# Kernel tuning notes

Hardware: AMD Instinct MI355X
Metric: run time of the kernel (lower is better)

Reference implementation:

```python
import jax, jax.numpy as jnp
import numpy as np

B, S, T = 16, 1024, 512
D, H, L, FF = 256, 8, 4, 1024
DH = D // H  # 32, even (RoPE requirement)


def setup_inputs() -> dict:
    key = jax.random.key(0)
    ks = jax.random.split(key, 8)
    n = lambda k, shape: jax.random.normal(k, shape, dtype=jnp.float32) * 0.02
    return {
        "x": jax.random.normal(ks[0], (B, S, T), dtype=jnp.float32),
        "tok_w": n(ks[1], (D, T)), "tok_b": jnp.zeros((D,), jnp.float32),
        "tnorm_g": jnp.ones((D,), jnp.float32), "tnorm_b": jnp.zeros((D,), jnp.float32),
        "in_proj_w": n(ks[2], (L, 3 * D, D)), "in_proj_b": jnp.zeros((L, 3 * D), jnp.float32),
        "out_w": n(ks[3], (L, D, D)), "out_b": jnp.zeros((L, D), jnp.float32),
        "ln1_g": jnp.ones((L, D), jnp.float32), "ln1_b": jnp.zeros((L, D), jnp.float32),
        "ln2_g": jnp.ones((L, D), jnp.float32), "ln2_b": jnp.zeros((L, D), jnp.float32),
        "lin1_w": n(ks[4], (L, FF, D)), "lin1_b": jnp.zeros((L, FF), jnp.float32),
        "lin2_w": n(ks[5], (L, D, FF)), "lin2_b": jnp.zeros((L, D), jnp.float32),
        "fnorm_g": jnp.ones((D,), jnp.float32), "fnorm_b": jnp.zeros((D,), jnp.float32),
    }


def _ln(x, g, b, eps=1e-5):
    m = x.mean(-1, keepdims=True)
    v = ((x - m) ** 2).mean(-1, keepdims=True)
    return (x - m) * jax.lax.rsqrt(v + eps) * g + b


def _rope_cache():
    half = DH // 2
    inv_freq = 1.0 / (10000.0 ** (jnp.arange(half, dtype=jnp.float32) / half))
    freqs = jnp.arange(S, dtype=jnp.float32)[:, None] * inv_freq[None, :]  # (S, half)
    cos = jnp.concatenate([jnp.cos(freqs), jnp.cos(freqs)], axis=-1)  # (S, DH)
    sin = jnp.concatenate([jnp.sin(freqs), jnp.sin(freqs)], axis=-1)
    return cos[None, None], sin[None, None]  # (1,1,S,DH)


def _rotate_half(x):
    x1, x2 = jnp.split(x, 2, axis=-1)
    return jnp.concatenate([-x2, x1], axis=-1)


def _rope(x, cos, sin):
    return x * cos + _rotate_half(x) * sin


def _encoder(x, tok_w, tok_b, tnorm_g, tnorm_b, in_proj_w, in_proj_b,
             out_w, out_b, ln1_g, ln1_b, ln2_g, ln2_b,
             lin1_w, lin1_b, lin2_w, lin2_b, fnorm_g, fnorm_b):
    # tokenize: Linear(T -> D) per sensor, then LayerNorm
    h = _ln(x @ tok_w.T + tok_b, tnorm_g, tnorm_b)  # (B,S,D)
    cos, sin = _rope_cache()
    scale = 1.0 / np.sqrt(DH).astype(np.float32)
    for i in range(L):
        # --- pre-norm RoPE self-attention ---
        y = _ln(h, ln1_g[i], ln1_b[i])
        qkv = y @ in_proj_w[i].T + in_proj_b[i]  # (B,S,3D)
        q, k, v = jnp.split(qkv, 3, axis=-1)
        q = q.reshape(B, S, H, DH).transpose(0, 2, 1, 3)  # (B,H,S,DH)
        k = k.reshape(B, S, H, DH).transpose(0, 2, 1, 3)
        v = v.reshape(B, S, H, DH).transpose(0, 2, 1, 3)
        q = _rope(q, cos, sin)
        k = _rope(k, cos, sin)
        attn = jax.nn.softmax(jnp.einsum('bhqd,bhkd->bhqk', q, k) * scale, axis=-1)
        o = jnp.einsum('bhqk,bhkd->bhqd', attn, v)
        o = o.transpose(0, 2, 1, 3).reshape(B, S, D)
        h = h + o @ out_w[i].T + out_b[i]
        # --- pre-norm FFN ---
        y2 = _ln(h, ln2_g[i], ln2_b[i])
        h = h + jax.nn.relu(y2 @ lin1_w[i].T + lin1_b[i]) @ lin2_w[i].T + lin2_b[i]
    return _ln(h, fnorm_g, fnorm_b)


def reference(x, tok_w, tok_b, tnorm_g, tnorm_b, in_proj_w, in_proj_b,
              out_w, out_b, ln1_g, ln1_b, ln2_g, ln2_b,
              lin1_w, lin1_b, lin2_w, lin2_b, fnorm_g, fnorm_b):
    return _encoder(x, tok_w, tok_b, tnorm_g, tnorm_b, in_proj_w, in_proj_b,
                    out_w, out_b, ln1_g, ln1_b, ln2_g, ln2_b,
                    lin1_w, lin1_b, lin2_w, lin2_b, fnorm_g, fnorm_b)
```

## Files before the change

kernel.cpp:

```cpp
#include <hip/hip_runtime.h>

#define BB 16
#define SS 1024
#define TT 512
#define DD 256
#define HH 8
#define LL 4
#define FFN 1024
#define DHH 32
#define MROWS (BB*SS)

typedef short bf16x8 __attribute__((ext_vector_type(8)));
typedef float f32x4 __attribute__((ext_vector_type(4)));
typedef float f32x2 __attribute__((ext_vector_type(2)));
typedef unsigned int u32x4 __attribute__((ext_vector_type(4)));

__device__ __forceinline__ unsigned short f2bf(float f) {
    unsigned int u = __float_as_uint(f);
    unsigned int r = (u + 0x7fffu + ((u >> 16) & 1u)) >> 16;
    return (unsigned short)r;
}
__device__ __forceinline__ float bf2f(unsigned short h) {
    return __uint_as_float(((unsigned int)h) << 16);
}
__device__ __forceinline__ unsigned int packbf(float a, float b) {
    return (__float_as_uint(a) >> 16) | (__float_as_uint(b) & 0xffff0000u);
}
__device__ __forceinline__ unsigned int packbf_perm(float p0, float p1) {
    return __builtin_amdgcn_perm(__float_as_uint(p1), __float_as_uint(p0), 0x07060302u);
}

__device__ __forceinline__ void g2l16(const unsigned short* g, unsigned short* l) {
    __builtin_amdgcn_global_load_lds(
        (const __attribute__((address_space(1))) unsigned int*)g,
        (__attribute__((address_space(3))) unsigned int*)l, 16, 0, 0);
}

__global__ __launch_bounds__(256) void convert_weights(
    const float* __restrict__ w0, const float* __restrict__ w1, const float* __restrict__ w2,
    const float* __restrict__ w3, const float* __restrict__ w4, unsigned short* __restrict__ dst)
{
    int i = blockIdx.x * 256 + threadIdx.x;
    if (i >= 3276800) return;
    float v;
    if (i < 131072)        v = w0[i];
    else if (i < 917504)   v = w1[i - 131072];
    else if (i < 1179648)  v = w2[i - 917504];
    else if (i < 2228224)  v = w3[i - 1179648];
    else                   v = w4[i - 2228224];
    dst[i] = f2bf(v);
}

__global__ __launch_bounds__(256) void convert_x(const float4* __restrict__ x, ushort4* __restrict__ xb, int n4)
{
    int i = blockIdx.x * 256 + threadIdx.x;
    if (i >= n4) return;
    float4 v = x[i];
    ushort4 o;
    o.x = f2bf(v.x); o.y = f2bf(v.y); o.z = f2bf(v.z); o.w = f2bf(v.w);
    xb[i] = o;
}

template<int BN, int RELU>
__global__ __launch_bounds__(256, 2) void gemm_lds(
    const unsigned short* __restrict__ A, const unsigned short* __restrict__ Bw,
    const float* __restrict__ bias, void* out, int M, int N, int K)
{
    constexpr int NJ = BN / 32;
    __shared__ __align__(16) unsigned short sA[2][128 * 32];
    __shared__ __align__(16) unsigned short sB[2][BN * 32];
    const int t = threadIdx.x;
    const int lane = t & 63, quad = lane >> 4, l16 = lane & 15;
    const int wave = t >> 6, wm = wave >> 1, wn = wave & 1;
    const int row0 = blockIdx.y * 128, col0 = blockIdx.x * BN;

    const unsigned short* gA = A + (size_t)(row0 + (t >> 2)) * K + (t & 3) * 8;
    const size_t rstep = (size_t)64 * K;
    const unsigned short* gBp[BN / 64];
    #pragma unroll
    for (int p = 0; p < BN / 64; ++p) {
        int l = p * 64 + (t >> 2);
        int wrow = (l & (16 * NJ)) + (l & 15) * NJ + ((l >> 4) & (NJ - 1));
        gBp[p] = Bw + (size_t)(col0 + wrow) * K + (t & 3) * 8;
    }

    f32x4 acc[4][NJ];
    #pragma unroll
    for (int i = 0; i < 4; ++i)
        #pragma unroll
        for (int j = 0; j < NJ; ++j)
            acc[i][j] = (f32x4){0.f, 0.f, 0.f, 0.f};

    g2l16(gA, &sA[0][t * 8]);
    g2l16(gA + rstep, &sA[0][(t + 256) * 8]);
    #pragma unroll
    for (int p = 0; p < BN / 64; ++p)
        g2l16(gBp[p], &sB[0][p * 2048 + t * 8]);

    for (int k0 = 0; k0 < K; k0 += 32) {
        const int cur = (k0 >> 5) & 1;
        __syncthreads();
        if (k0 + 32 < K) {
            const int nxt = cur ^ 1;
            g2l16(gA + k0 + 32, &sA[nxt][t * 8]);
            g2l16(gA + rstep + k0 + 32, &sA[nxt][(t + 256) * 8]);
            #pragma unroll
            for (int p = 0; p < BN / 64; ++p)
                g2l16(gBp[p] + k0 + 32, &sB[nxt][p * 2048 + t * 8]);
        }
        bf16x8 a[4], b[NJ];
        #pragma unroll
        for (int i = 0; i < 4; ++i)
            a[i] = *(const bf16x8*)(&sA[cur][(wm * 64 + i * 16 + l16) * 32 + quad * 8]);
        #pragma unroll
        for (int j = 0; j < NJ; ++j)
            b[j] = *(const bf16x8*)(&sB[cur][(wn * (BN / 2) + j * 16 + l16) * 32 + quad * 8]);
        #pragma unroll
        for (int i = 0; i < 4; ++i)
            #pragma unroll
            for (int j = 0; j < NJ; ++j)
                acc[i][j] = __builtin_amdgcn_mfma_f32_16x16x32_bf16(a[i], b[j], acc[i][j], 0, 0, 0);
    }

    const int colbase = col0 + wn * (BN / 2) + l16 * NJ;
    float bb[NJ];
    #pragma unroll
    for (int j = 0; j < NJ; ++j) bb[j] = bias[colbase + j];
    #pragma unroll
    for (int i = 0; i < 4; ++i) {
        #pragma unroll
        for (int r = 0; r < 4; ++r) {
            int row = row0 + wm * 64 + i * 16 + quad * 4 + r;
            float v[NJ];
            #pragma unroll
            for (int j = 0; j < NJ; ++j) {
                v[j] = acc[i][j][r] + bb[j];
                if (RELU) v[j] = fmaxf(v[j], 0.f);
            }
            unsigned short* dst = (unsigned short*)out + (size_t)row * N + colbase;
            if constexpr (NJ == 4) {
                uint2 w; w.x = packbf(v[0], v[1]); w.y = packbf(v[2], v[3]);
                *(uint2*)dst = w;
            } else {
                uint4 w; w.x = packbf(v[0], v[1]); w.y = packbf(v[2], v[3]);
                w.z = packbf(v[4], v[5]); w.w = packbf(v[6], v[7]);
                *(uint4*)dst = w;
            }
        }
    }
}

template<int RESID, int LNH, int YF32>
__global__ __launch_bounds__(512, 2) void gemm_row(
    const unsigned short* __restrict__ A, const unsigned short* __restrict__ Bw,
    const float* __restrict__ bias, const float* __restrict__ resid,
    float* __restrict__ hout, void* __restrict__ yout,
    const float* __restrict__ gh, const float* __restrict__ bh,
    const float* __restrict__ gy, const float* __restrict__ by, int K)
{
    __shared__ __align__(16) unsigned short sA[2][64 * 32];
    __shared__ __align__(16) unsigned short sB[2][256 * 32];
    __shared__ float2 part[2][64][4];
    const int t = threadIdx.x;
    const int quad = (t >> 4) & 3, l16 = t & 15;
    const int wave = t >> 6, wm = wave >> 2, wn = wave & 3;
    const int row0 = blockIdx.x * 64;

    const unsigned short* gA = A + (size_t)(row0 + ((t >> 2) & 63)) * K + (t & 3) * 8;
    const int l0 = t >> 2, l1 = 128 + l0;
    const unsigned short* gB0 = Bw + (size_t)((l0 & 192) + (l0 & 15) * 4 + ((l0 >> 4) & 3)) * K + (t & 3) * 8;
    const unsigned short* gB1 = Bw + (size_t)((l1 & 192) + (l1 & 15) * 4 + ((l1 >> 4) & 3)) * K + (t & 3) * 8;

    f32x4 acc[2][4];
    #pragma unroll
    for (int i = 0; i < 2; ++i)
        #pragma unroll
        for (int j = 0; j < 4; ++j)
            acc[i][j] = (f32x4){0.f, 0.f, 0.f, 0.f};

    auto stage = [&](int k0, int buf) {
        if (t < 256) g2l16(gA + k0, &sA[buf][t * 8]);
        g2l16(gB0 + k0, &sB[buf][t * 8]);
        g2l16(gB1 + k0, &sB[buf][(t + 512) * 8]);
    };

    stage(0, 0);
    for (int k0 = 0; k0 < K; k0 += 32) {
        const int cur = (k0 >> 5) & 1;
        __syncthreads();
        if (k0 + 32 < K) stage(k0 + 32, cur ^ 1);
        bf16x8 a[2], b[4];
        #pragma unroll
        for (int i = 0; i < 2; ++i)
            a[i] = *(const bf16x8*)(&sA[cur][(wm * 32 + i * 16 + l16) * 32 + quad * 8]);
        #pragma unroll
        for (int j = 0; j < 4; ++j)
            b[j] = *(const bf16x8*)(&sB[cur][(wn * 64 + j * 16 + l16) * 32 + quad * 8]);
        #pragma unroll
        for (int i = 0; i < 2; ++i)
            #pragma unroll
            for (int j = 0; j < 4; ++j)
                acc[i][j] = __builtin_amdgcn_mfma_f32_16x16x32_bf16(a[i], b[j], acc[i][j], 0, 0, 0);
    }

    const int colbase = wn * 64 + l16 * 4;
    const float4 bb = *(const float4*)(bias + colbase);
    #pragma unroll
    for (int i = 0; i < 2; ++i) {
        #pragma unroll
        for (int r = 0; r < 4; ++r) {
            const int rl = wm * 32 + i * 16 + quad * 4 + r;
            float v0 = acc[i][0][r] + bb.x;
            float v1 = acc[i][1][r] + bb.y;
            float v2 = acc[i][2][r] + bb.z;
            float v3 = acc[i][3][r] + bb.w;
            if (RESID) {
                float4 rv = *(const float4*)(resid + (size_t)(row0 + rl) * DD + colbase);
                v0 += rv.x; v1 += rv.y; v2 += rv.z; v3 += rv.w;
            }
            acc[i][0][r] = v0; acc[i][1][r] = v1; acc[i][2][r] = v2; acc[i][3][r] = v3;
            float s = v0 + v1 + v2 + v3;
            float ss = v0 * v0 + v1 * v1 + v2 * v2 + v3 * v3;
            #pragma unroll
            for (int m = 1; m <= 8; m <<= 1) { s += __shfl_xor(s, m); ss += __shfl_xor(ss, m); }
            if (l16 == 0) part[0][rl][wn] = (float2){s, ss};
        }
    }
    __syncthreads();

    float4 gyv = *(const float4*)(gy + colbase);
    float4 byv = *(const float4*)(by + colbase);
    float4 ghv = {0.f, 0.f, 0.f, 0.f}, bhv = {0.f, 0.f, 0.f, 0.f};
    if (LNH) { ghv = *(const float4*)(gh + colbase); bhv = *(const float4*)(bh + colbase); }

    #pragma unroll
    for (int i = 0; i < 2; ++i) {
        #pragma unroll
        for (int r = 0; r < 4; ++r) {
            const int rl = wm * 32 + i * 16 + quad * 4 + r;
            float2 p0 = part[0][rl][0], p1 = part[0][rl][1], p2 = part[0][rl][2], p3 = part[0][rl][3];
            float mean = (p0.x + p1.x + p2.x + p3.x) * (1.f / 256.f);
            float var  = (p0.y + p1.y + p2.y + p3.y) * (1.f / 256.f) - mean * mean;
            float inv  = rsqrtf(var + 1e-5f);
            float h0, h1, h2, h3;
            if (LNH) {
                h0 = (acc[i][0][r] - mean) * inv * ghv.x + bhv.x;
                h1 = (acc[i][1][r] - mean) * inv * ghv.y + bhv.y;
                h2 = (acc[i][2][r] - mean) * inv * ghv.z + bhv.z;
                h3 = (acc[i][3][r] - mean) * inv * ghv.w + bhv.w;
            } else {
                h0 = acc[i][0][r]; h1 = acc[i][1][r]; h2 = acc[i][2][r]; h3 = acc[i][3][r];
            }
            if (!YF32)
                *(float4*)(hout + (size_t)(row0 + rl) * DD + colbase) = (float4){h0, h1, h2, h3};
            if (LNH) {
                acc[i][0][r] = h0; acc[i][1][r] = h1; acc[i][2][r] = h2; acc[i][3][r] = h3;
                float s = h0 + h1 + h2 + h3;
                float ss = h0 * h0 + h1 * h1 + h2 * h2 + h3 * h3;
                #pragma unroll
                for (int m = 1; m <= 8; m <<= 1) { s += __shfl_xor(s, m); ss += __shfl_xor(ss, m); }
                if (l16 == 0) part[1][rl][wn] = (float2){s, ss};
            } else {
                float y0 = (h0 - mean) * inv * gyv.x + byv.x;
                float y1 = (h1 - mean) * inv * gyv.y + byv.y;
                float y2 = (h2 - mean) * inv * gyv.z + byv.z;
                float y3 = (h3 - mean) * inv * gyv.w + byv.w;
                if (YF32) {
                    *(float4*)((float*)yout + (size_t)(row0 + rl) * DD + colbase) = (float4){y0, y1, y2, y3};
                } else {
                    uint2 w; w.x = packbf(y0, y1); w.y = packbf(y2, y3);
                    *(uint2*)((unsigned short*)yout + (size_t)(row0 + rl) * DD + colbase) = w;
                }
            }
        }
    }

    if (LNH) {
        __syncthreads();
        #pragma unroll
        for (int i = 0; i < 2; ++i) {
            #pragma unroll
            for (int r = 0; r < 4; ++r) {
                const int rl = wm * 32 + i * 16 + quad * 4 + r;
                float2 p0 = part[1][rl][0], p1 = part[1][rl][1], p2 = part[1][rl][2], p3 = part[1][rl][3];
                float mean = (p0.x + p1.x + p2.x + p3.x) * (1.f / 256.f);
                float var  = (p0.y + p1.y + p2.y + p3.y) * (1.f / 256.f) - mean * mean;
                float inv  = rsqrtf(var + 1e-5f);
                float y0 = (acc[i][0][r] - mean) * inv * gyv.x + byv.x;
                float y1 = (acc[i][1][r] - mean) * inv * gyv.y + byv.y;
                float y2 = (acc[i][2][r] - mean) * inv * gyv.z + byv.z;
                float y3 = (acc[i][3][r] - mean) * inv * gyv.w + byv.w;
                uint2 w; w.x = packbf(y0, y1); w.y = packbf(y2, y3);
                *(uint2*)((unsigned short*)yout + (size_t)(row0 + rl) * DD + colbase) = w;
            }
        }
    }
}

__global__ __launch_bounds__(512) void rope_kernel(const unsigned short* __restrict__ qkv,
    unsigned short* __restrict__ qr, unsigned short* __restrict__ kr, unsigned short* __restrict__ vt)
{
    __shared__ float scc[64 * 16], scs[64 * 16];
    __shared__ unsigned short vlds[256 * 68];
    const int t = threadIdx.x;
    const int r0 = blockIdx.x * 64;
    const int b = r0 >> 10, s0 = r0 & 1023;

    #pragma unroll
    for (int e2 = 0; e2 < 2; ++e2) {
        int e = t * 2 + e2;
        int rl = e >> 4, jj = e & 15;
        float ivf = __expf(-(float)jj * 0.575646273248511f);
        float c, sn;
        __sincosf((float)(s0 + rl) * ivf, &sn, &c);
        scc[rl * 16 + jj] = c;
        scs[rl * 16 + jj] = sn;
    }
    __syncthreads();

    const int sub = t >> 8, i = t & 255;
    const int h = i >> 5, d = i & 31, j = d & 15;
    const int bh = (b << 3) | h;
    const float qscale = 1.4426950408889634f / 5.656854249492381f;
    for (int it = 0; it < 32; ++it) {
        int rl = it * 2 + sub;
        int s = s0 + rl;
        const unsigned short* rp = qkv + (size_t)(r0 + rl) * 768;
        float qv = bf2f(rp[i]);
        float kv = bf2f(rp[256 + i]);
        float vv = bf2f(rp[512 + i]);
        float c = scc[rl * 16 + j], sn = scs[rl * 16 + j];
        float qp = __shfl_xor(qv, 16);
        float kp = __shfl_xor(kv, 16);
        float rq = (qv * c + ((d < 16) ? -qp : qp) * sn) * qscale;
        float rk = kv * c + ((d < 16) ? -kp : kp) * sn;
        qr[((size_t)bh * SS + s) * DHH + d] = f2bf(rq);
        int jj2 = s & 31;
        int sp = (s & ~31) | (((jj2 & 1) << 4) | (jj2 >> 1));
        kr[((size_t)bh * SS + sp) * DHH + d] = f2bf(rk);
        vlds[i * 68 + rl] = f2bf(vv);
    }
    __syncthreads();

    const int wave = t >> 6, lane = t & 63;
    for (int p = 0; p < 32; ++p) {
        int row = p * 8 + wave;
        int hh = row >> 5, dd = row & 31;
        unsigned short v = vlds[row * 68 + lane];
        vt[((size_t)((b << 3) | hh) * DHH + dd) * SS + s0 + lane] = v;
    }
}

__global__ __launch_bounds__(128, 2) void attn_kernel(
    const unsigned short* __restrict__ qr, const unsigned short* __restrict__ kr,
    const unsigned short* __restrict__ vt, unsigned short* __restrict__ ob)
{
    int t = threadIdx.x;
    int lane = t & 63, wave = t >> 6;
    int quad = (lane >> 4), l16 = lane & 15;
    int bid = blockIdx.x;
    int xcd = bid & 7, jb = bid >> 3;
    int gid = jb * 2 + wave;
    int bh = xcd * 16 + (gid >> 4);
    int q0 = (gid & 15) * 64;
    int b = bh >> 3, h = bh & 7;
    const unsigned short* qbase = qr + ((size_t)bh * SS + q0) * DHH;
    const unsigned short* kbase = kr + (size_t)bh * SS * DHH;
    const unsigned short* vbase = vt + (size_t)bh * DHH * SS;
    bf16x8 qa[4];
    #pragma unroll
    for (int qt = 0; qt < 4; ++qt)
        qa[qt] = *(const bf16x8*)(qbase + (size_t)(qt * 16 + l16) * DHH + quad * 8);
    f32x4 o[4][2] = {};
    f32x2 lsum[4] = {};

    bf16x8 kbA[2][2], vbA[2][2], kbB[2][2], vbB[2][2];

    auto loadKV = [&](int k0, bf16x8 (&kb)[2][2], bf16x8 (&vb)[2][2]) {
        #pragma unroll
        for (int kc = 0; kc < 2; ++kc) {
            const unsigned short* kp = kbase + (size_t)(k0 + kc * 32) * DHH;
            kb[kc][0] = *(const bf16x8*)(kp + (size_t)l16 * DHH + quad * 8);
            kb[kc][1] = *(const bf16x8*)(kp + (size_t)(16 + l16) * DHH + quad * 8);
            vb[kc][0] = *(const bf16x8*)(vbase + (size_t)l16 * SS + k0 + kc * 32 + quad * 8);
            vb[kc][1] = *(const bf16x8*)(vbase + (size_t)(l16 + 16) * SS + k0 + kc * 32 + quad * 8);
        }
    };

    auto tile = [&](bf16x8 (&kb)[2][2], bf16x8 (&vb)[2][2]) {
        __builtin_amdgcn_s_setprio(1);
        #pragma unroll
        for (int qt = 0; qt < 4; ++qt)
            #pragma unroll
            for (int kc = 0; kc < 2; ++kc) {
                f32x4 z = {0.f, 0.f, 0.f, 0.f};
                f32x4 s0 = __builtin_amdgcn_mfma_f32_16x16x32_bf16(kb[kc][0], qa[qt], z, 0, 0, 0);
                f32x4 s1 = __builtin_amdgcn_mfma_f32_16x16x32_bf16(kb[kc][1], qa[qt], z, 0, 0, 0);
                u32x4 pw;
                #pragma unroll
                for (int r = 0; r < 4; ++r) {
                    float p0 = __builtin_amdgcn_exp2f(s0[r]);
                    float p1 = __builtin_amdgcn_exp2f(s1[r]);
                    lsum[qt] += (f32x2){p0, p1};
                    pw[r] = packbf_perm(p0, p1);
                }
                bf16x8 pa = __builtin_bit_cast(bf16x8, pw);
                o[qt][0] = __builtin_amdgcn_mfma_f32_16x16x32_bf16(pa, vb[kc][0], o[qt][0], 0, 0, 0);
                o[qt][1] = __builtin_amdgcn_mfma_f32_16x16x32_bf16(pa, vb[kc][1], o[qt][1], 0, 0, 0);
            }
        __builtin_amdgcn_s_setprio(0);
    };

    loadKV(0, kbA, vbA);
    for (int k0 = 0; k0 < SS; k0 += 128) {
        loadKV(k0 + 64, kbB, vbB);
        tile(kbA, vbA);
        if (k0 + 128 < SS) loadKV(k0 + 128, kbA, vbA);
        tile(kbB, vbB);
    }

    #pragma unroll
    for (int qt = 0; qt < 4; ++qt) {
        float s = lsum[qt][0] + lsum[qt][1];
        s += __shfl_xor(s, 16);
        s += __shfl_xor(s, 32);
        float inv = 1.f / s;
        #pragma unroll
        for (int r = 0; r < 4; ++r) {
            float invr = __shfl(inv, quad * 4 + r);
            int qrow = q0 + qt * 16 + quad * 4 + r;
            size_t base = ((size_t)b * SS + qrow) * DD + h * DHH;
            ob[base + l16]      = f2bf(o[qt][0][r] * invr);
            ob[base + 16 + l16] = f2bf(o[qt][1][r] * invr);
        }
    }
}

extern "C" void kernel_launch(void* const* d_in, const int* in_sizes, int n_in,
                              void* d_out, int out_size, void* d_ws, size_t ws_size,
                              hipStream_t stream)
{
    const float* x        = (const float*)d_in[0];
    const float* tok_w    = (const float*)d_in[1];
    const float* tok_b    = (const float*)d_in[2];
    const float* tnorm_g  = (const float*)d_in[3];
    const float* tnorm_b  = (const float*)d_in[4];
    const float* in_proj_w= (const float*)d_in[5];
    const float* in_proj_b= (const float*)d_in[6];
    const float* out_w    = (const float*)d_in[7];
    const float* out_b    = (const float*)d_in[8];
    const float* ln1_g    = (const float*)d_in[9];
    const float* ln1_b    = (const float*)d_in[10];
    const float* ln2_g    = (const float*)d_in[11];
    const float* ln2_b    = (const float*)d_in[12];
    const float* lin1_w   = (const float*)d_in[13];
    const float* lin1_b   = (const float*)d_in[14];
    const float* lin2_w   = (const float*)d_in[15];
    const float* lin2_b   = (const float*)d_in[16];
    const float* fnorm_g  = (const float*)d_in[17];
    const float* fnorm_b  = (const float*)d_in[18];

    char* ws = (char*)d_ws;
    unsigned short* wb        = (unsigned short*)ws;
    unsigned short* wb_tok    = wb;
    unsigned short* wb_inproj = wb + 131072;
    unsigned short* wb_out    = wb + 917504;
    unsigned short* wb_lin1   = wb + 1179648;
    unsigned short* wb_lin2   = wb + 2228224;
    unsigned short* qkvb = (unsigned short*)(ws + 6553600);
    unsigned short* xb   = qkvb;
    float*          h    = (float*)(ws + 31719424);
    unsigned short* y    = (unsigned short*)(ws + 48496640);
    unsigned short* qr   = (unsigned short*)(ws + 56885248);
    unsigned short* kr   = (unsigned short*)(ws + 65273856);
    unsigned short* vt   = (unsigned short*)(ws + 73662464);
    unsigned short* ob   = (unsigned short*)(ws + 82051072);
    unsigned short* a1   = (unsigned short*)(ws + 90439680);

    convert_weights<<<dim3(12800), dim3(256), 0, stream>>>(tok_w, in_proj_w, out_w, lin1_w, lin2_w, wb);
    convert_x<<<dim3(8192), dim3(256), 0, stream>>>((const float4*)x, (ushort4*)xb, MROWS * TT / 4);

    gemm_row<0, 1, 0><<<dim3(MROWS / 64), dim3(512), 0, stream>>>(
        xb, wb_tok, tok_b, nullptr, h, y, tnorm_g, tnorm_b, ln1_g, ln1_b, TT);

    for (int i = 0; i < LL; ++i) {
        gemm_lds<128, 0><<<dim3((3 * DD) / 128, MROWS / 128), dim3(256), 0, stream>>>(
            y, wb_inproj + (size_t)i * 3 * DD * DD, in_proj_b + i * 3 * DD, qkvb, MROWS, 3 * DD, DD);
        rope_kernel<<<dim3(MROWS / 64), dim3(512), 0, stream>>>(qkvb, qr, kr, vt);
        attn_kernel<<<dim3(1024), dim3(128), 0, stream>>>(qr, kr, vt, ob);
        gemm_row<1, 0, 0><<<dim3(MROWS / 64), dim3(512), 0, stream>>>(
            ob, wb_out + (size_t)i * DD * DD, out_b + i * DD, h, h, y,
            nullptr, nullptr, ln2_g + i * DD, ln2_b + i * DD, DD);
        gemm_lds<256, 1><<<dim3(FFN / 256, MROWS / 128), dim3(256), 0, stream>>>(
            y, wb_lin1 + (size_t)i * FFN * DD, lin1_b + i * FFN, a1, MROWS, FFN, DD);
        if (i < LL - 1) {
            gemm_row<1, 0, 0><<<dim3(MROWS / 64), dim3(512), 0, stream>>>(
                a1, wb_lin2 + (size_t)i * DD * FFN, lin2_b + i * DD, h, h, y,
                nullptr, nullptr, ln1_g + (i + 1) * DD, ln1_b + (i + 1) * DD, FFN);
        } else {
            gemm_row<1, 0, 1><<<dim3(MROWS / 64), dim3(512), 0, stream>>>(
                a1, wb_lin2 + (size_t)i * DD * FFN, lin2_b + i * DD, h, h, d_out,
                nullptr, nullptr, fnorm_g, fnorm_b, FFN);
        }
    }
}
```

Baseline: 608.2 us.

## Fuse RoPE and head-layout scatter into the QKV projection GEMM epilogue

Replaces the separate QKV GEMM plus rope_kernel with a single gemm_qkv kernel. Its B-row permutation lets each lane hold a RoPE pair partner reachable by a shuffle, and the epilogue writes rotated, scaled Q, permuted K and transposed V directly. This removes the write and re-read of the 16k x 768 bf16 qkv buffer and one launch per layer. In exchange the V transpose is now written with strided global stores instead of through LDS, and the GEMM carries extra shared memory for sin/cos tables.

```diff
diff --git a/kernel.cpp b/kernel.cpp
--- a/kernel.cpp
+++ b/kernel.cpp
@@ -145,6 +145,144 @@
                 uint4 w; w.x = packbf(v[0], v[1]); w.y = packbf(v[2], v[3]);
                 w.z = packbf(v[4], v[5]); w.w = packbf(v[6], v[7]);
                 *(uint4*)dst = w;
+            }
+        }
+    }
+}
+
+__global__ __launch_bounds__(256, 2) void gemm_qkv(
+    const unsigned short* __restrict__ A, const unsigned short* __restrict__ Bw,
+    const float* __restrict__ bias,
+    unsigned short* __restrict__ qr, unsigned short* __restrict__ kr,
+    unsigned short* __restrict__ vt)
+{
+    constexpr int K = 256;
+    __shared__ __align__(16) unsigned short sA[2][128 * 32];
+    __shared__ __align__(16) unsigned short sB[2][128 * 32];
+    __shared__ float scc[128 * 20], scs[128 * 20];
+    const int t = threadIdx.x;
+    const int lane = t & 63, quad = lane >> 4, l16 = lane & 15;
+    const int wave = t >> 6, wm = wave >> 1, wn = wave & 1;
+    const int row0 = blockIdx.y * 128, col0 = blockIdx.x * 128;
+    const int sec = blockIdx.x >> 1;
+    const int b = row0 >> 10, s0 = row0 & 1023;
+
+    if (sec < 2) {
+        #pragma unroll
+        for (int k = 0; k < 8; ++k) {
+            int e = t * 8 + k;
+            int rl = e >> 4, jj = e & 15;
+            float ivf = __expf(-(float)jj * 0.575646273248511f);
+            float c, sn;
+            __sincosf((float)(s0 + rl) * ivf, &sn, &c);
+            scc[rl * 20 + jj] = c;
+            scs[rl * 20 + jj] = sn;
+        }
+    }
+
+    const unsigned short* gA = A + (size_t)(row0 + (t >> 2)) * K + (t & 3) * 8;
+    const size_t rstep = (size_t)64 * K;
+    const unsigned short* gBp[2];
+    #pragma unroll
+    for (int p = 0; p < 2; ++p) {
+        int l = p * 64 + (t >> 2);
+        int wrow = (l & 64) + (l & 15) * 4 + ((l >> 4) & 3);
+        gBp[p] = Bw + (size_t)(col0 + wrow) * K + (t & 3) * 8;
+    }
+
+    f32x4 acc[4][4];
+    #pragma unroll
+    for (int i = 0; i < 4; ++i)
+        #pragma unroll
+        for (int j = 0; j < 4; ++j)
+            acc[i][j] = (f32x4){0.f, 0.f, 0.f, 0.f};
+
+    g2l16(gA, &sA[0][t * 8]);
+    g2l16(gA + rstep, &sA[0][(t + 256) * 8]);
+    #pragma unroll
+    for (int p = 0; p < 2; ++p)
+        g2l16(gBp[p], &sB[0][p * 2048 + t * 8]);
+
+    for (int k0 = 0; k0 < K; k0 += 32) {
+        const int cur = (k0 >> 5) & 1;
+        __syncthreads();
+        if (k0 + 32 < K) {
+            const int nxt = cur ^ 1;
+            g2l16(gA + k0 + 32, &sA[nxt][t * 8]);
+            g2l16(gA + rstep + k0 + 32, &sA[nxt][(t + 256) * 8]);
+            #pragma unroll
+            for (int p = 0; p < 2; ++p)
+                g2l16(gBp[p] + k0 + 32, &sB[nxt][p * 2048 + t * 8]);
+        }
+        bf16x8 a[4], bfr[4];
+        #pragma unroll
+        for (int i = 0; i < 4; ++i)
+            a[i] = *(const bf16x8*)(&sA[cur][(wm * 64 + i * 16 + l16) * 32 + quad * 8]);
+        #pragma unroll
+        for (int j = 0; j < 4; ++j)
+            bfr[j] = *(const bf16x8*)(&sB[cur][(wn * 64 + j * 16 + l16) * 32 + quad * 8]);
+        #pragma unroll
+        for (int i = 0; i < 4; ++i)
+            #pragma unroll
+            for (int j = 0; j < 4; ++j)
+                acc[i][j] = __builtin_amdgcn_mfma_f32_16x16x32_bf16(a[i], bfr[j], acc[i][j], 0, 0, 0);
+    }
+
+    const int gcol = col0 + wn * 64 + l16 * 4;
+    const int cc = gcol & 255;
+    const int h = cc >> 5, d0v = cc & 31, j0 = d0v & 15;
+    const int bh = (b << 3) | h;
+    float bbv[4];
+    *(float4*)bbv = *(const float4*)(bias + gcol);
+
+    if (sec < 2) {
+        const float sgn = ((l16 & 4) == 0) ? -1.f : 1.f;
+        const float qs = 1.4426950408889634f / 5.656854249492381f;
+        #pragma unroll
+        for (int i = 0; i < 4; ++i) {
+            #pragma unroll
+            for (int r = 0; r < 4; ++r) {
+                const int rl = wm * 64 + i * 16 + quad * 4 + r;
+                float v0 = acc[i][0][r] + bbv[0];
+                float v1 = acc[i][1][r] + bbv[1];
+                float v2 = acc[i][2][r] + bbv[2];
+                float v3 = acc[i][3][r] + bbv[3];
+                float p0 = __shfl_xor(v0, 4);
+                float p1 = __shfl_xor(v1, 4);
+                float p2 = __shfl_xor(v2, 4);
+                float p3 = __shfl_xor(v3, 4);
+                float4 cv = *(const float4*)(&scc[rl * 20 + j0]);
+                float4 sv = *(const float4*)(&scs[rl * 20 + j0]);
+                float o0 = v0 * cv.x + sgn * p0 * sv.x;
+                float o1 = v1 * cv.y + sgn * p1 * sv.y;
+                float o2 = v2 * cv.z + sgn * p2 * sv.z;
+                float o3 = v3 * cv.w + sgn * p3 * sv.w;
+                const int s = s0 + rl;
+                uint2 w;
+                if (sec == 0) {
+                    o0 *= qs; o1 *= qs; o2 *= qs; o3 *= qs;
+                    w.x = packbf(o0, o1); w.y = packbf(o2, o3);
+                    *(uint2*)(qr + ((size_t)bh * SS + s) * DHH + d0v) = w;
+                } else {
+                    int jj2 = s & 31;
+                    int sp = (s & ~31) | (((jj2 & 1) << 4) | (jj2 >> 1));
+                    w.x = packbf(o0, o1); w.y = packbf(o2, o3);
+                    *(uint2*)(kr + ((size_t)bh * SS + sp) * DHH + d0v) = w;
+                }
+            }
+        }
+    } else {
+        #pragma unroll
+        for (int i = 0; i < 4; ++i) {
+            const int sbase = s0 + wm * 64 + i * 16 + quad * 4;
+            #pragma unroll
+            for (int j = 0; j < 4; ++j) {
+                float w0 = acc[i][j][0] + bbv[j];
+                float w1 = acc[i][j][1] + bbv[j];
+                float w2 = acc[i][j][2] + bbv[j];
+                float w3 = acc[i][j][3] + bbv[j];
+                uint2 w; w.x = packbf(w0, w1); w.y = packbf(w2, w3);
+                *(uint2*)(vt + ((size_t)bh * DHH + d0v + j) * SS + sbase) = w;
             }
         }
     }
@@ -297,60 +435,6 @@
     }
 }
 
-__global__ __launch_bounds__(512) void rope_kernel(const unsigned short* __restrict__ qkv,
-    unsigned short* __restrict__ qr, unsigned short* __restrict__ kr, unsigned short* __restrict__ vt)
-{
-    __shared__ float scc[64 * 16], scs[64 * 16];
-    __shared__ unsigned short vlds[256 * 68];
-    const int t = threadIdx.x;
-    const int r0 = blockIdx.x * 64;
-    const int b = r0 >> 10, s0 = r0 & 1023;
-
-    #pragma unroll
-    for (int e2 = 0; e2 < 2; ++e2) {
-        int e = t * 2 + e2;
-        int rl = e >> 4, jj = e & 15;
-        float ivf = __expf(-(float)jj * 0.575646273248511f);
-        float c, sn;
-        __sincosf((float)(s0 + rl) * ivf, &sn, &c);
-        scc[rl * 16 + jj] = c;
-        scs[rl * 16 + jj] = sn;
-    }
-    __syncthreads();
-
-    const int sub = t >> 8, i = t & 255;
-    const int h = i >> 5, d = i & 31, j = d & 15;
-    const int bh = (b << 3) | h;
-    const float qscale = 1.4426950408889634f / 5.656854249492381f;
-    for (int it = 0; it < 32; ++it) {
-        int rl = it * 2 + sub;
-        int s = s0 + rl;
-        const unsigned short* rp = qkv + (size_t)(r0 + rl) * 768;
-        float qv = bf2f(rp[i]);
-        float kv = bf2f(rp[256 + i]);
-        float vv = bf2f(rp[512 + i]);
-        float c = scc[rl * 16 + j], sn = scs[rl * 16 + j];
-        float qp = __shfl_xor(qv, 16);
-        float kp = __shfl_xor(kv, 16);
-        float rq = (qv * c + ((d < 16) ? -qp : qp) * sn) * qscale;
-        float rk = kv * c + ((d < 16) ? -kp : kp) * sn;
-        qr[((size_t)bh * SS + s) * DHH + d] = f2bf(rq);
-        int jj2 = s & 31;
-        int sp = (s & ~31) | (((jj2 & 1) << 4) | (jj2 >> 1));
-        kr[((size_t)bh * SS + sp) * DHH + d] = f2bf(rk);
-        vlds[i * 68 + rl] = f2bf(vv);
-    }
-    __syncthreads();
-
-    const int wave = t >> 6, lane = t & 63;
-    for (int p = 0; p < 32; ++p) {
-        int row = p * 8 + wave;
-        int hh = row >> 5, dd = row & 31;
-        unsigned short v = vlds[row * 68 + lane];
-        vt[((size_t)((b << 3) | hh) * DHH + dd) * SS + s0 + lane] = v;
-    }
-}
-
 __global__ __launch_bounds__(128, 2) void attn_kernel(
     const unsigned short* __restrict__ qr, const unsigned short* __restrict__ kr,
     const unsigned short* __restrict__ vt, unsigned short* __restrict__ ob)
@@ -467,8 +551,7 @@
     unsigned short* wb_out    = wb + 917504;
     unsigned short* wb_lin1   = wb + 1179648;
     unsigned short* wb_lin2   = wb + 2228224;
-    unsigned short* qkvb = (unsigned short*)(ws + 6553600);
-    unsigned short* xb   = qkvb;
+    unsigned short* xb   = (unsigned short*)(ws + 6553600);
     float*          h    = (float*)(ws + 31719424);
     unsigned short* y    = (unsigned short*)(ws + 48496640);
     unsigned short* qr   = (unsigned short*)(ws + 56885248);
@@ -484,9 +567,8 @@
         xb, wb_tok, tok_b, nullptr, h, y, tnorm_g, tnorm_b, ln1_g, ln1_b, TT);
 
     for (int i = 0; i < LL; ++i) {
-        gemm_lds<128, 0><<<dim3((3 * DD) / 128, MROWS / 128), dim3(256), 0, stream>>>(
-            y, wb_inproj + (size_t)i * 3 * DD * DD, in_proj_b + i * 3 * DD, qkvb, MROWS, 3 * DD, DD);
-        rope_kernel<<<dim3(MROWS / 64), dim3(512), 0, stream>>>(qkvb, qr, kr, vt);
+        gemm_qkv<<<dim3(6, MROWS / 128), dim3(256), 0, stream>>>(
+            y, wb_inproj + (size_t)i * 3 * DD * DD, in_proj_b + i * 3 * DD, qr, kr, vt);
         attn_kernel<<<dim3(1024), dim3(128), 0, stream>>>(qr, kr, vt, ob);
         gemm_row<1, 0, 0><<<dim3(MROWS / 64), dim3(512), 0, stream>>>(
             ob, wb_out + (size_t)i * DD * DD, out_b + i * DD, h, h, y,
```

Result: faster. 582.2 us (-4.3%).
